# Performance work log

Hardware: AMD Instinct MI355X
Metric: run time of the kernel (lower is better)

The kernel has to match this reference:

```python
import jax, jax.numpy as jnp
import numpy as np

NUM_CLASS = 22  # restypes_with_x_and_gap: 20 AAs + 'X' + '-' (gap is last)


def layer_norm(x, g, b, eps=1e-5):
    mu = jnp.mean(x, axis=-1, keepdims=True)
    var = jnp.var(x, axis=-1, keepdims=True)
    return (x - mu) * jax.lax.rsqrt(var + eps) * g + b


def setup_inputs() -> dict:
    key = jax.random.key(0)
    ks = jax.random.split(key, 8)
    B, M, N, DS, DP = 1, 128, 256, 384, 128
    C = NUM_CLASS
    s = 0.02
    return dict(
        single=jax.random.normal(ks[0], (B, N, DS), dtype=jnp.float32),
        pair=jax.random.normal(ks[1], (B, N, N, DP), dtype=jnp.float32),
        msa=jax.random.randint(ks[2], (B, M, N), 0, C),
        w1=jax.random.normal(ks[3], (DS, DS), dtype=jnp.float32) * s,
        b1=jnp.zeros((DS,), jnp.float32),
        g1=jnp.ones((DS,), jnp.float32),
        be1=jnp.zeros((DS,), jnp.float32),
        w2=jax.random.normal(ks[4], (DS, C), dtype=jnp.float32) * s,
        b2=jnp.zeros((C,), jnp.float32),
        g2=jnp.ones((DP,), jnp.float32),
        be2=jnp.zeros((DP,), jnp.float32),
        w3=jax.random.normal(ks[5], (DP, C * C), dtype=jnp.float32) * s,
        b3=jnp.zeros((C * C,), jnp.float32),
    )


def reference(single, pair, msa, w1, b1, g1, be1, w2, b2, g2, be2, w3, b3):
    C = NUM_CLASS
    B, N = single.shape[0], single.shape[1]
    # make_mask(restypes_with_x_and_gap, '-'): 1 everywhere except the gap class (last index)
    label_mask = jnp.ones((C,), single.dtype).at[C - 1].set(0.0)

    # single branch: Linear -> GELU(exact) -> LayerNorm -> Linear
    h = jax.nn.gelu(single @ w1 + b1, approximate=False)
    ei = layer_norm(h, g1, be1) @ w2 + b2  # [B, N, C]

    # pairwise branch: symmetrize -> LayerNorm -> Linear -> ReLU, zero diagonal
    zsym = (pair + jnp.swapaxes(pair, 1, 2)) * 0.5
    eij = jax.nn.relu(layer_norm(zsym, g2, be2) @ w3 + b3)  # [B, N, N, C*C]
    eij = eij * (1.0 - jnp.eye(N, dtype=eij.dtype))[:, :, None]

    # coevolution logits: one-hot MSA (with gap class masked) contracted with pairwise couplings
    eijcd = eij.reshape(B, N, N, C, C)
    oh = jax.nn.one_hot(msa, C, dtype=eij.dtype) * label_mask  # [B, M, N, C] fold mask 'd' into one-hot
    hi = jnp.einsum('bmjd,bijcd->bmic', oh, eijcd)  # [B, M, N, C]
    logits = ei[:, None] + hi  # [B, M, N, C]
    return eij, ei, logits
```

## Files before the change

### kernel.cpp

```cpp
#include <hip/hip_runtime.h>
#include <hip/hip_bf16.h>

#define NN 256
#define MM 128
#define DS 384
#define DP 128
#define CC 22
#define C2 484

#define OUT_EI  (NN*NN*C2)
#define OUT_LOG (OUT_EI + NN*CC)

typedef __attribute__((ext_vector_type(8))) short short8;
typedef __attribute__((ext_vector_type(4))) float f32x4;

__device__ __forceinline__ unsigned f2bf(float x) {
  unsigned u = __float_as_uint(x);
  return (u + 0x7FFFu + ((u >> 16) & 1u)) >> 16;
}

__global__ void k_w3pack(const float* __restrict__ w3, int4* __restrict__ w3f) {
  int ct = blockIdx.x, kt = blockIdx.y, l = threadIdx.x;
  int c = ct * 16 + (l & 15);
  int kb = kt * 32 + (l >> 4) * 8;
  unsigned v[8];
#pragma unroll
  for (int e = 0; e < 8; ++e) {
    float x = (c < C2) ? w3[(kb + e) * C2 + c] : 0.f;
    v[e] = f2bf(x);
  }
  int4 pk;
  pk.x = (int)(v[0] | (v[1] << 16));
  pk.y = (int)(v[2] | (v[3] << 16));
  pk.z = (int)(v[4] | (v[5] << 16));
  pk.w = (int)(v[6] | (v[7] << 16));
  w3f[(kt * 31 + ct) * 64 + l] = pk;
}

__global__ void k_msat(const int* __restrict__ msa, unsigned char* __restrict__ mt) {
  int j = blockIdx.x, m = threadIdx.x;
  mt[j * MM + m] = (unsigned char)msa[m * NN + j];
}

__global__ __launch_bounds__(384) void k_single(
    const float* __restrict__ single, const float* __restrict__ w1,
    const float* __restrict__ b1, const float* __restrict__ g1,
    const float* __restrict__ be1, const float* __restrict__ w2,
    const float* __restrict__ b2, float* __restrict__ out_ei,
    float* __restrict__ out_log)
{
  __shared__ float srow[DS];
  __shared__ float hlx[DS];
  __shared__ float part[16 * CC];
  __shared__ float wred[8], wredq[8], mur[2];
  int n = blockIdx.x, t = threadIdx.x;
  srow[t] = single[n * DS + t];
  for (int idx = t; idx < MM * CC; idx += 384) {
    int m = idx / CC, c = idx - m * CC;
    out_log[(m * NN + n) * CC + c] = 0.f;
  }
  __syncthreads();
  float acc = b1[t];
#pragma unroll 8
  for (int d = 0; d < DS; ++d) acc = fmaf(srow[d], w1[d * DS + t], acc);
  float hv = 0.5f * acc * (1.0f + erff(acc * 0.70710678118654752f));
  float s = hv, q = hv * hv;
#pragma unroll
  for (int off = 32; off; off >>= 1) { s += __shfl_xor(s, off); q += __shfl_xor(q, off); }
  if ((t & 63) == 0) { wred[t >> 6] = s; wredq[t >> 6] = q; }
  __syncthreads();
  if (t == 0) {
    float S = 0.f, Q = 0.f;
    for (int w = 0; w < 6; ++w) { S += wred[w]; Q += wredq[w]; }
    float mu = S / (float)DS;
    mur[0] = mu; mur[1] = rsqrtf(Q / (float)DS - mu * mu + 1e-5f);
  }
  __syncthreads();
  hlx[t] = (hv - mur[0]) * mur[1] * g1[t] + be1[t];
  __syncthreads();
  if (t < 352) {
    int g = t / CC, c = t - g * CC;
    float p = 0.f;
#pragma unroll
    for (int k = g * 24; k < g * 24 + 24; ++k) p = fmaf(hlx[k], w2[k * CC + c], p);
    part[t] = p;
  }
  __syncthreads();
  if (t < CC) {
    float sm = b2[t];
#pragma unroll
    for (int g = 0; g < 16; ++g) sm += part[g * CC + t];
    out_ei[n * CC + t] = sm;
  }
}

__global__ __launch_bounds__(512, 4) void k_fused(
    const float* __restrict__ pair, const unsigned char* __restrict__ msa_tb,
    const float* __restrict__ g2, const float* __restrict__ be2,
    const float* __restrict__ b3, const int4* __restrict__ w3f,
    const float* __restrict__ ei,
    float* __restrict__ out_eij, float* __restrict__ out_log)
{
  __shared__ __align__(16) char smem[64512];
  unsigned char* msa_s = (unsigned char*)(smem + 52224);
  char* zln = smem + 56320;

  const int i = blockIdx.x, jh = blockIdx.y;
  const int t = threadIdx.x;
  const int w = t >> 6, l = t & 63;
  const int lr = l & 15, lg = l >> 4;

  for (int idx = t; idx < 52224 / 4; idx += 512) ((unsigned*)smem)[idx] = 0u;

  f32x4 acc[2];
  acc[0] = (f32x4){0.f, 0.f, 0.f, 0.f};
  acc[1] = (f32x4){0.f, 0.f, 0.f, 0.f};

  const float2 g2v = ((const float2*)g2)[l];
  const float2 bev = ((const float2*)be2)[l];
  const short8* w3fv = (const short8*)w3f;

  __syncthreads();

  for (int ch = 0; ch < 4; ++ch) {
    const int j0 = jh * 128 + ch * 32;

#pragma unroll
    for (int it = 0; it < 4; ++it) {
      int jl = w * 4 + it;
      int j = j0 + jl;
      float2 a = ((const float2*)(pair + (i * NN + j) * DP))[l];
      float2 b = ((const float2*)(pair + (j * NN + i) * DP))[l];
      float zx = 0.5f * (a.x + b.x), zy = 0.5f * (a.y + b.y);
      float s = zx + zy, q = zx * zx + zy * zy;
#pragma unroll
      for (int off = 32; off; off >>= 1) { s += __shfl_xor(s, off); q += __shfl_xor(q, off); }
      float mu = s * (1.f / 128.f);
      float rs = rsqrtf(q * (1.f / 128.f) - mu * mu + 1e-5f);
      float nx = (zx - mu) * rs * g2v.x + bev.x;
      float ny = (zy - mu) * rs * g2v.y + bev.y;
      unsigned pk = f2bf(nx) | (f2bf(ny) << 16);
      int blk = (l >> 2) ^ (jl & 15);
      *(unsigned*)(zln + jl * 256 + blk * 16 + (l & 3) * 4) = pk;
    }
    ((uint2*)msa_s)[t] = ((const uint2*)(msa_tb + j0 * MM))[t];
    __syncthreads();

    short8 a0[4], a1[4];
#pragma unroll
    for (int kt = 0; kt < 4; ++kt) {
      a0[kt] = *(const short8*)(zln + lr * 256 + (((kt * 4 + lg) ^ lr) * 16));
      a1[kt] = *(const short8*)(zln + (16 + lr) * 256 + (((kt * 4 + lg) ^ lr) * 16));
    }
    for (int ct = w; ct < 31; ct += 8) {
      f32x4 c0 = {0.f, 0.f, 0.f, 0.f}, c1 = {0.f, 0.f, 0.f, 0.f};
#pragma unroll
      for (int kt = 0; kt < 4; ++kt) {
        short8 bfr = w3fv[(kt * 31 + ct) * 64 + l];
        c0 = __builtin_amdgcn_mfma_f32_16x16x32_bf16(a0[kt], bfr, c0, 0, 0, 0);
        c1 = __builtin_amdgcn_mfma_f32_16x16x32_bf16(a1[kt], bfr, c1, 0, 0, 0);
      }
      int cflat = ct * 16 + lr;
      if (cflat < C2) {
        float bias = b3[cflat];
        int cdiv = cflat / CC;
        int dd = cflat - cdiv * CC;
#pragma unroll
        for (int r = 0; r < 4; ++r) {
          int jjl0 = lg * 4 + r;
          int j = j0 + jjl0;
          float v = fmaxf(c0[r] + bias, 0.f);
          if (j == i) v = 0.f;
          out_eij[(i * NN + j) * C2 + cflat] = v;
          *(unsigned short*)(smem + jjl0 * 1584 + cdiv * 72 + dd * 2) = (unsigned short)f2bf(v);

          int jjl1 = 16 + lg * 4 + r;
          j = j0 + jjl1;
          v = fmaxf(c1[r] + bias, 0.f);
          if (j == i) v = 0.f;
          out_eij[(i * NN + j) * C2 + cflat] = v;
          *(unsigned short*)(smem + jjl1 * 1584 + cdiv * 72 + dd * 2) = (unsigned short)f2bf(v);
        }
      }
    }
    __syncthreads();

    for (int jj = 0; jj < 32; ++jj) {
      int s = msa_s[jj * 128 + w * 16 + lr];
      int rel = s - lg * 8;
      unsigned hval = (s != 21 && ((unsigned)rel) < 8u) ? (0x3F80u << ((rel & 1) << 4)) : 0u;
      int word = rel >> 1;
      union { short8 s8; unsigned u[4]; } bu;
      bu.u[0] = (word == 0) ? hval : 0u;
      bu.u[1] = (word == 1) ? hval : 0u;
      bu.u[2] = (word == 2) ? hval : 0u;
      bu.u[3] = (word == 3) ? hval : 0u;
#pragma unroll
      for (int cp = 0; cp < 2; ++cp) {
        short8 af = *(const short8*)(smem + jj * 1584 + (cp * 16 + lr) * 72 + lg * 16);
        acc[cp] = __builtin_amdgcn_mfma_f32_16x16x32_bf16(af, bu.s8, acc[cp], 0, 0, 0);
      }
    }
    __syncthreads();
  }

  {
    int m = w * 16 + lr;
#pragma unroll
    for (int cp = 0; cp < 2; ++cp) {
#pragma unroll
      for (int r = 0; r < 4; ++r) {
        int c = cp * 16 + lg * 4 + r;
        if (c < CC) {
          float add = acc[cp][r] + (jh == 0 ? ei[i * CC + c] : 0.f);
          atomicAdd(&out_log[(m * NN + i) * CC + c], add);
        }
      }
    }
  }
}

extern "C" void kernel_launch(void* const* d_in, const int* in_sizes, int n_in,
                              void* d_out, int out_size, void* d_ws, size_t ws_size,
                              hipStream_t stream) {
  const float* single = (const float*)d_in[0];
  const float* pairp  = (const float*)d_in[1];
  const int*   msa    = (const int*)d_in[2];
  const float* w1  = (const float*)d_in[3];
  const float* b1  = (const float*)d_in[4];
  const float* g1  = (const float*)d_in[5];
  const float* be1 = (const float*)d_in[6];
  const float* w2  = (const float*)d_in[7];
  const float* b2  = (const float*)d_in[8];
  const float* g2  = (const float*)d_in[9];
  const float* be2 = (const float*)d_in[10];
  const float* w3  = (const float*)d_in[11];
  const float* b3  = (const float*)d_in[12];

  float* out = (float*)d_out;
  float* out_eij = out;
  float* out_ei  = out + OUT_EI;
  float* out_log = out + OUT_LOG;

  int4* w3f = (int4*)d_ws;
  unsigned char* msa_tb = (unsigned char*)d_ws + 131072;

  hipLaunchKernelGGL(k_w3pack, dim3(31, 4), dim3(64), 0, stream, w3, w3f);
  hipLaunchKernelGGL(k_msat, dim3(NN), dim3(MM), 0, stream, msa, msa_tb);
  hipLaunchKernelGGL(k_single, dim3(NN), dim3(384), 0, stream,
                     single, w1, b1, g1, be1, w2, b2, out_ei, out_log);
  hipLaunchKernelGGL(k_fused, dim3(256, 2), dim3(512), 0, stream,
                     pairp, msa_tb, g2, be2, b3, (const int4*)w3f,
                     out_ei, out_eij, out_log);
}
```

Measured before the change: 273.8 us.

## Split fused kernel into smaller 256-thread blocks over j quarters and merge prep kernels

The fused pairwise kernel now processes 32 j-columns per block in 16-row chunks with 4 waves, on a 256x8 grid instead of 256x2 with 512 threads. The eij staging buffer is compacted, and the einsum stage is reorganised so each wave covers two MSA row tiles. The w3 packing and MSA transpose kernels are merged into one launch. The aim is better occupancy, smaller LDS use and one fewer launch, at the cost of more atomic adds on the logits and fewer reuses of each w3 fragment per block.

```diff
diff --git a/kernel.cpp b/kernel.cpp
--- a/kernel.cpp
+++ b/kernel.cpp
@@ -11,6 +11,10 @@
 #define OUT_EI  (NN*NN*C2)
 #define OUT_LOG (OUT_EI + NN*CC)
 
+#define ZSTRJ 1056
+#define ZE_END (16*ZSTRJ + 512)
+#define LDS_TOTAL (ZE_END + 2048)
+
 typedef __attribute__((ext_vector_type(8))) short short8;
 typedef __attribute__((ext_vector_type(4))) float f32x4;
 
@@ -19,27 +23,27 @@
   return (u + 0x7FFFu + ((u >> 16) & 1u)) >> 16;
 }
 
-__global__ void k_w3pack(const float* __restrict__ w3, int4* __restrict__ w3f) {
-  int ct = blockIdx.x, kt = blockIdx.y, l = threadIdx.x;
-  int c = ct * 16 + (l & 15);
-  int kb = kt * 32 + (l >> 4) * 8;
-  unsigned v[8];
-#pragma unroll
-  for (int e = 0; e < 8; ++e) {
-    float x = (c < C2) ? w3[(kb + e) * C2 + c] : 0.f;
-    v[e] = f2bf(x);
-  }
-  int4 pk;
-  pk.x = (int)(v[0] | (v[1] << 16));
-  pk.y = (int)(v[2] | (v[3] << 16));
-  pk.z = (int)(v[4] | (v[5] << 16));
-  pk.w = (int)(v[6] | (v[7] << 16));
-  w3f[(kt * 31 + ct) * 64 + l] = pk;
-}
-
-__global__ void k_msat(const int* __restrict__ msa, unsigned char* __restrict__ mt) {
-  int j = blockIdx.x, m = threadIdx.x;
-  mt[j * MM + m] = (unsigned char)msa[m * NN + j];
+__global__ __launch_bounds__(128) void k_prep(
+    const float* __restrict__ w3, const int* __restrict__ msa,
+    int4* __restrict__ w3f, unsigned char* __restrict__ mt)
+{
+  int b = blockIdx.x, t = threadIdx.x;
+  mt[b * MM + t] = (unsigned char)msa[t * NN + b];
+  if (b < 124 && t < 64) {
+    int ct = b % 31, kt = b / 31, l = t;
+    int c = ct * 16 + (l & 15);
+    int kb = kt * 32 + (l >> 4) * 8;
+    unsigned v[8];
+#pragma unroll
+    for (int e = 0; e < 8; ++e)
+      v[e] = (c < C2) ? f2bf(w3[(kb + e) * C2 + c]) : 0u;
+    int4 pk;
+    pk.x = (int)(v[0] | (v[1] << 16));
+    pk.y = (int)(v[2] | (v[3] << 16));
+    pk.z = (int)(v[4] | (v[5] << 16));
+    pk.w = (int)(v[6] | (v[7] << 16));
+    w3f[(kt * 31 + ct) * 64 + l] = pk;
+  }
 }
 
 __global__ __launch_bounds__(384) void k_single(
@@ -94,36 +98,36 @@
   }
 }
 
-__global__ __launch_bounds__(512, 4) void k_fused(
+__global__ __launch_bounds__(256, 6) void k_fused(
     const float* __restrict__ pair, const unsigned char* __restrict__ msa_tb,
     const float* __restrict__ g2, const float* __restrict__ be2,
     const float* __restrict__ b3, const int4* __restrict__ w3f,
     const float* __restrict__ ei,
     float* __restrict__ out_eij, float* __restrict__ out_log)
 {
-  __shared__ __align__(16) char smem[64512];
-  unsigned char* msa_s = (unsigned char*)(smem + 52224);
-  char* zln = smem + 56320;
-
-  const int i = blockIdx.x, jh = blockIdx.y;
+  __shared__ __align__(16) char smem[LDS_TOTAL];
+  unsigned char* msa_s = (unsigned char*)(smem + ZE_END);
+
+  const int i = blockIdx.x, jq = blockIdx.y;
   const int t = threadIdx.x;
   const int w = t >> 6, l = t & 63;
   const int lr = l & 15, lg = l >> 4;
 
-  for (int idx = t; idx < 52224 / 4; idx += 512) ((unsigned*)smem)[idx] = 0u;
-
-  f32x4 acc[2];
-  acc[0] = (f32x4){0.f, 0.f, 0.f, 0.f};
-  acc[1] = (f32x4){0.f, 0.f, 0.f, 0.f};
+  for (int idx = t; idx < LDS_TOTAL / 4; idx += 256) ((unsigned*)smem)[idx] = 0u;
+
+  f32x4 acc[2][2];
+#pragma unroll
+  for (int a_ = 0; a_ < 2; ++a_)
+#pragma unroll
+    for (int b_ = 0; b_ < 2; ++b_) acc[a_][b_] = (f32x4){0.f, 0.f, 0.f, 0.f};
 
   const float2 g2v = ((const float2*)g2)[l];
   const float2 bev = ((const float2*)be2)[l];
   const short8* w3fv = (const short8*)w3f;
-
-  __syncthreads();
-
-  for (int ch = 0; ch < 4; ++ch) {
-    const int j0 = jh * 128 + ch * 32;
+  __syncthreads();
+
+  for (int ch = 0; ch < 2; ++ch) {
+    const int j0 = jq * 32 + ch * 16;
 
 #pragma unroll
     for (int it = 0; it < 4; ++it) {
@@ -140,26 +144,28 @@
       float nx = (zx - mu) * rs * g2v.x + bev.x;
       float ny = (zy - mu) * rs * g2v.y + bev.y;
       unsigned pk = f2bf(nx) | (f2bf(ny) << 16);
-      int blk = (l >> 2) ^ (jl & 15);
-      *(unsigned*)(zln + jl * 256 + blk * 16 + (l & 3) * 4) = pk;
+      int blk = (l >> 2) ^ jl;
+      *(unsigned*)(smem + jl * 256 + blk * 16 + (l & 3) * 4) = pk;
     }
     ((uint2*)msa_s)[t] = ((const uint2*)(msa_tb + j0 * MM))[t];
     __syncthreads();
 
-    short8 a0[4], a1[4];
-#pragma unroll
-    for (int kt = 0; kt < 4; ++kt) {
-      a0[kt] = *(const short8*)(zln + lr * 256 + (((kt * 4 + lg) ^ lr) * 16));
-      a1[kt] = *(const short8*)(zln + (16 + lr) * 256 + (((kt * 4 + lg) ^ lr) * 16));
-    }
-    for (int ct = w; ct < 31; ct += 8) {
-      f32x4 c0 = {0.f, 0.f, 0.f, 0.f}, c1 = {0.f, 0.f, 0.f, 0.f};
-#pragma unroll
-      for (int kt = 0; kt < 4; ++kt) {
-        short8 bfr = w3fv[(kt * 31 + ct) * 64 + l];
-        c0 = __builtin_amdgcn_mfma_f32_16x16x32_bf16(a0[kt], bfr, c0, 0, 0, 0);
-        c1 = __builtin_amdgcn_mfma_f32_16x16x32_bf16(a1[kt], bfr, c1, 0, 0, 0);
-      }
+    short8 afr[4];
+#pragma unroll
+    for (int kt = 0; kt < 4; ++kt)
+      afr[kt] = *(const short8*)(smem + lr * 256 + (((kt * 4 + lg) ^ lr) * 16));
+    __syncthreads();
+
+    for (int ct = w; ct < 31; ct += 4) {
+      short8 bf0 = w3fv[(0 * 31 + ct) * 64 + l];
+      short8 bf1 = w3fv[(1 * 31 + ct) * 64 + l];
+      short8 bf2 = w3fv[(2 * 31 + ct) * 64 + l];
+      short8 bf3 = w3fv[(3 * 31 + ct) * 64 + l];
+      f32x4 cc2 = {0.f, 0.f, 0.f, 0.f};
+      cc2 = __builtin_amdgcn_mfma_f32_16x16x32_bf16(afr[0], bf0, cc2, 0, 0, 0);
+      cc2 = __builtin_amdgcn_mfma_f32_16x16x32_bf16(afr[1], bf1, cc2, 0, 0, 0);
+      cc2 = __builtin_amdgcn_mfma_f32_16x16x32_bf16(afr[2], bf2, cc2, 0, 0, 0);
+      cc2 = __builtin_amdgcn_mfma_f32_16x16x32_bf16(afr[3], bf3, cc2, 0, 0, 0);
       int cflat = ct * 16 + lr;
       if (cflat < C2) {
         float bias = b3[cflat];
@@ -167,52 +173,59 @@
         int dd = cflat - cdiv * CC;
 #pragma unroll
         for (int r = 0; r < 4; ++r) {
-          int jjl0 = lg * 4 + r;
-          int j = j0 + jjl0;
-          float v = fmaxf(c0[r] + bias, 0.f);
+          int jl = lg * 4 + r, j = j0 + jl;
+          float v = fmaxf(cc2[r] + bias, 0.f);
           if (j == i) v = 0.f;
           out_eij[(i * NN + j) * C2 + cflat] = v;
-          *(unsigned short*)(smem + jjl0 * 1584 + cdiv * 72 + dd * 2) = (unsigned short)f2bf(v);
-
-          int jjl1 = 16 + lg * 4 + r;
-          j = j0 + jjl1;
-          v = fmaxf(c1[r] + bias, 0.f);
-          if (j == i) v = 0.f;
-          out_eij[(i * NN + j) * C2 + cflat] = v;
-          *(unsigned short*)(smem + jjl1 * 1584 + cdiv * 72 + dd * 2) = (unsigned short)f2bf(v);
+          *(unsigned short*)(smem + jl * ZSTRJ + cdiv * 48 + dd * 2) = (unsigned short)f2bf(v);
         }
       }
     }
     __syncthreads();
 
-    for (int jj = 0; jj < 32; ++jj) {
-      int s = msa_s[jj * 128 + w * 16 + lr];
-      int rel = s - lg * 8;
-      unsigned hval = (s != 21 && ((unsigned)rel) < 8u) ? (0x3F80u << ((rel & 1) << 4)) : 0u;
-      int word = rel >> 1;
-      union { short8 s8; unsigned u[4]; } bu;
-      bu.u[0] = (word == 0) ? hval : 0u;
-      bu.u[1] = (word == 1) ? hval : 0u;
-      bu.u[2] = (word == 2) ? hval : 0u;
-      bu.u[3] = (word == 3) ? hval : 0u;
+#pragma unroll 4
+    for (int jj = 0; jj < 16; ++jj) {
+      int s0 = msa_s[jj * 128 + w * 16 + lr];
+      int s1 = msa_s[jj * 128 + (w + 4) * 16 + lr];
+      union { short8 s8; unsigned u[4]; } b0, b1;
+      {
+        int rel = s0 - lg * 8;
+        unsigned hval = (s0 != 21 && ((unsigned)rel) < 8u) ? (0x3F80u << ((rel & 1) << 4)) : 0u;
+        int word = rel >> 1;
+        b0.u[0] = (word == 0) ? hval : 0u;
+        b0.u[1] = (word == 1) ? hval : 0u;
+        b0.u[2] = (word == 2) ? hval : 0u;
+        b0.u[3] = (word == 3) ? hval : 0u;
+      }
+      {
+        int rel = s1 - lg * 8;
+        unsigned hval = (s1 != 21 && ((unsigned)rel) < 8u) ? (0x3F80u << ((rel & 1) << 4)) : 0u;
+        int word = rel >> 1;
+        b1.u[0] = (word == 0) ? hval : 0u;
+        b1.u[1] = (word == 1) ? hval : 0u;
+        b1.u[2] = (word == 2) ? hval : 0u;
+        b1.u[3] = (word == 3) ? hval : 0u;
+      }
 #pragma unroll
       for (int cp = 0; cp < 2; ++cp) {
-        short8 af = *(const short8*)(smem + jj * 1584 + (cp * 16 + lr) * 72 + lg * 16);
-        acc[cp] = __builtin_amdgcn_mfma_f32_16x16x32_bf16(af, bu.s8, acc[cp], 0, 0, 0);
-      }
-    }
-    __syncthreads();
-  }
-
-  {
-    int m = w * 16 + lr;
+        short8 af = *(const short8*)(smem + jj * ZSTRJ + (cp * 16 + lr) * 48 + lg * 16);
+        acc[0][cp] = __builtin_amdgcn_mfma_f32_16x16x32_bf16(af, b0.s8, acc[0][cp], 0, 0, 0);
+        acc[1][cp] = __builtin_amdgcn_mfma_f32_16x16x32_bf16(af, b1.s8, acc[1][cp], 0, 0, 0);
+      }
+    }
+    __syncthreads();
+  }
+
+#pragma unroll
+  for (int mt = 0; mt < 2; ++mt) {
+    int m = (mt * 4 + w) * 16 + lr;
 #pragma unroll
     for (int cp = 0; cp < 2; ++cp) {
 #pragma unroll
       for (int r = 0; r < 4; ++r) {
         int c = cp * 16 + lg * 4 + r;
         if (c < CC) {
-          float add = acc[cp][r] + (jh == 0 ? ei[i * CC + c] : 0.f);
+          float add = acc[mt][cp][r] + (jq == 0 ? ei[i * CC + c] : 0.f);
           atomicAdd(&out_log[(m * NN + i) * CC + c], add);
         }
       }
@@ -245,11 +258,10 @@
   int4* w3f = (int4*)d_ws;
   unsigned char* msa_tb = (unsigned char*)d_ws + 131072;
 
-  hipLaunchKernelGGL(k_w3pack, dim3(31, 4), dim3(64), 0, stream, w3, w3f);
-  hipLaunchKernelGGL(k_msat, dim3(NN), dim3(MM), 0, stream, msa, msa_tb);
+  hipLaunchKernelGGL(k_prep, dim3(NN), dim3(128), 0, stream, w3, msa, w3f, msa_tb);
   hipLaunchKernelGGL(k_single, dim3(NN), dim3(384), 0, stream,
                      single, w1, b1, g1, be1, w2, b2, out_ei, out_log);
-  hipLaunchKernelGGL(k_fused, dim3(256, 2), dim3(512), 0, stream,
+  hipLaunchKernelGGL(k_fused, dim3(256, 8), dim3(256), 0, stream,
                      pairp, msa_tb, g2, be2, b3, (const int4*)w3f,
                      out_ei, out_eij, out_log);
 }
```

After: 396.4 us. 44.8% more time.

## Shrink fused-kernel LDS by aliasing staging buffers and merge prep kernels

Applied to the files above, without the earlier changes.

The fused kernel now reuses one LDS region for both the normalized pair tile and the bf16 coupling staging tile. A barrier after the A-fragment loads makes the reuse safe, and the coupling row stride drops from 72 to 48 bytes. Together these cut shared memory from about 64 KB to about 38 KB per block, so more blocks can fit on each CU. The two small prep kernels (w3 packing and MSA transpose) become one launch, the w3 fragment loads are hoisted ahead of the MFMAs, and the one-hot contraction loop is unrolled. The tighter stride means MFMA reads run past each valid row into neighbouring data. This relies on zero one-hot weights and discarded padding channels to stay correct.

```diff
diff --git a/kernel.cpp b/kernel.cpp
--- a/kernel.cpp
+++ b/kernel.cpp
@@ -11,6 +11,11 @@
 #define OUT_EI  (NN*NN*C2)
 #define OUT_LOG (OUT_EI + NN*CC)
 
+#define ZSTRJ 1056
+#define ZE_BYTES (32*ZSTRJ)
+#define ZE_END (ZE_BYTES + 512)
+#define LDS_TOTAL (ZE_END + 4096)
+
 typedef __attribute__((ext_vector_type(8))) short short8;
 typedef __attribute__((ext_vector_type(4))) float f32x4;
 
@@ -19,27 +24,27 @@
   return (u + 0x7FFFu + ((u >> 16) & 1u)) >> 16;
 }
 
-__global__ void k_w3pack(const float* __restrict__ w3, int4* __restrict__ w3f) {
-  int ct = blockIdx.x, kt = blockIdx.y, l = threadIdx.x;
-  int c = ct * 16 + (l & 15);
-  int kb = kt * 32 + (l >> 4) * 8;
-  unsigned v[8];
-#pragma unroll
-  for (int e = 0; e < 8; ++e) {
-    float x = (c < C2) ? w3[(kb + e) * C2 + c] : 0.f;
-    v[e] = f2bf(x);
-  }
-  int4 pk;
-  pk.x = (int)(v[0] | (v[1] << 16));
-  pk.y = (int)(v[2] | (v[3] << 16));
-  pk.z = (int)(v[4] | (v[5] << 16));
-  pk.w = (int)(v[6] | (v[7] << 16));
-  w3f[(kt * 31 + ct) * 64 + l] = pk;
-}
-
-__global__ void k_msat(const int* __restrict__ msa, unsigned char* __restrict__ mt) {
-  int j = blockIdx.x, m = threadIdx.x;
-  mt[j * MM + m] = (unsigned char)msa[m * NN + j];
+__global__ __launch_bounds__(128) void k_prep(
+    const float* __restrict__ w3, const int* __restrict__ msa,
+    int4* __restrict__ w3f, unsigned char* __restrict__ mt)
+{
+  int b = blockIdx.x, t = threadIdx.x;
+  mt[b * MM + t] = (unsigned char)msa[t * NN + b];
+  if (b < 124 && t < 64) {
+    int ct = b % 31, kt = b / 31, l = t;
+    int c = ct * 16 + (l & 15);
+    int kb = kt * 32 + (l >> 4) * 8;
+    unsigned v[8];
+#pragma unroll
+    for (int e = 0; e < 8; ++e)
+      v[e] = (c < C2) ? f2bf(w3[(kb + e) * C2 + c]) : 0u;
+    int4 pk;
+    pk.x = (int)(v[0] | (v[1] << 16));
+    pk.y = (int)(v[2] | (v[3] << 16));
+    pk.z = (int)(v[4] | (v[5] << 16));
+    pk.w = (int)(v[6] | (v[7] << 16));
+    w3f[(kt * 31 + ct) * 64 + l] = pk;
+  }
 }
 
 __global__ __launch_bounds__(384) void k_single(
@@ -101,16 +106,15 @@
     const float* __restrict__ ei,
     float* __restrict__ out_eij, float* __restrict__ out_log)
 {
-  __shared__ __align__(16) char smem[64512];
-  unsigned char* msa_s = (unsigned char*)(smem + 52224);
-  char* zln = smem + 56320;
+  __shared__ __align__(16) char smem[LDS_TOTAL];
+  unsigned char* msa_s = (unsigned char*)(smem + ZE_END);
 
   const int i = blockIdx.x, jh = blockIdx.y;
   const int t = threadIdx.x;
   const int w = t >> 6, l = t & 63;
   const int lr = l & 15, lg = l >> 4;
 
-  for (int idx = t; idx < 52224 / 4; idx += 512) ((unsigned*)smem)[idx] = 0u;
+  for (int idx = t; idx < LDS_TOTAL / 4; idx += 512) ((unsigned*)smem)[idx] = 0u;
 
   f32x4 acc[2];
   acc[0] = (f32x4){0.f, 0.f, 0.f, 0.f};
@@ -119,7 +123,6 @@
   const float2 g2v = ((const float2*)g2)[l];
   const float2 bev = ((const float2*)be2)[l];
   const short8* w3fv = (const short8*)w3f;
-
   __syncthreads();
 
   for (int ch = 0; ch < 4; ++ch) {
@@ -141,7 +144,7 @@
       float ny = (zy - mu) * rs * g2v.y + bev.y;
       unsigned pk = f2bf(nx) | (f2bf(ny) << 16);
       int blk = (l >> 2) ^ (jl & 15);
-      *(unsigned*)(zln + jl * 256 + blk * 16 + (l & 3) * 4) = pk;
+      *(unsigned*)(smem + jl * 256 + blk * 16 + (l & 3) * 4) = pk;
     }
     ((uint2*)msa_s)[t] = ((const uint2*)(msa_tb + j0 * MM))[t];
     __syncthreads();
@@ -149,17 +152,25 @@
     short8 a0[4], a1[4];
 #pragma unroll
     for (int kt = 0; kt < 4; ++kt) {
-      a0[kt] = *(const short8*)(zln + lr * 256 + (((kt * 4 + lg) ^ lr) * 16));
-      a1[kt] = *(const short8*)(zln + (16 + lr) * 256 + (((kt * 4 + lg) ^ lr) * 16));
-    }
+      a0[kt] = *(const short8*)(smem + lr * 256 + (((kt * 4 + lg) ^ lr) * 16));
+      a1[kt] = *(const short8*)(smem + (16 + lr) * 256 + (((kt * 4 + lg) ^ lr) * 16));
+    }
+    __syncthreads();
+
     for (int ct = w; ct < 31; ct += 8) {
+      short8 bf0 = w3fv[(0 * 31 + ct) * 64 + l];
+      short8 bf1 = w3fv[(1 * 31 + ct) * 64 + l];
+      short8 bf2 = w3fv[(2 * 31 + ct) * 64 + l];
+      short8 bf3 = w3fv[(3 * 31 + ct) * 64 + l];
       f32x4 c0 = {0.f, 0.f, 0.f, 0.f}, c1 = {0.f, 0.f, 0.f, 0.f};
-#pragma unroll
-      for (int kt = 0; kt < 4; ++kt) {
-        short8 bfr = w3fv[(kt * 31 + ct) * 64 + l];
-        c0 = __builtin_amdgcn_mfma_f32_16x16x32_bf16(a0[kt], bfr, c0, 0, 0, 0);
-        c1 = __builtin_amdgcn_mfma_f32_16x16x32_bf16(a1[kt], bfr, c1, 0, 0, 0);
-      }
+      c0 = __builtin_amdgcn_mfma_f32_16x16x32_bf16(a0[0], bf0, c0, 0, 0, 0);
+      c0 = __builtin_amdgcn_mfma_f32_16x16x32_bf16(a0[1], bf1, c0, 0, 0, 0);
+      c0 = __builtin_amdgcn_mfma_f32_16x16x32_bf16(a0[2], bf2, c0, 0, 0, 0);
+      c0 = __builtin_amdgcn_mfma_f32_16x16x32_bf16(a0[3], bf3, c0, 0, 0, 0);
+      c1 = __builtin_amdgcn_mfma_f32_16x16x32_bf16(a1[0], bf0, c1, 0, 0, 0);
+      c1 = __builtin_amdgcn_mfma_f32_16x16x32_bf16(a1[1], bf1, c1, 0, 0, 0);
+      c1 = __builtin_amdgcn_mfma_f32_16x16x32_bf16(a1[2], bf2, c1, 0, 0, 0);
+      c1 = __builtin_amdgcn_mfma_f32_16x16x32_bf16(a1[3], bf3, c1, 0, 0, 0);
       int cflat = ct * 16 + lr;
       if (cflat < C2) {
         float bias = b3[cflat];
@@ -167,24 +178,24 @@
         int dd = cflat - cdiv * CC;
 #pragma unroll
         for (int r = 0; r < 4; ++r) {
-          int jjl0 = lg * 4 + r;
-          int j = j0 + jjl0;
+          int jl0 = lg * 4 + r, j = j0 + jl0;
           float v = fmaxf(c0[r] + bias, 0.f);
           if (j == i) v = 0.f;
           out_eij[(i * NN + j) * C2 + cflat] = v;
-          *(unsigned short*)(smem + jjl0 * 1584 + cdiv * 72 + dd * 2) = (unsigned short)f2bf(v);
-
-          int jjl1 = 16 + lg * 4 + r;
-          j = j0 + jjl1;
+          *(unsigned short*)(smem + jl0 * ZSTRJ + cdiv * 48 + dd * 2) = (unsigned short)f2bf(v);
+
+          int jl1 = 16 + lg * 4 + r;
+          j = j0 + jl1;
           v = fmaxf(c1[r] + bias, 0.f);
           if (j == i) v = 0.f;
           out_eij[(i * NN + j) * C2 + cflat] = v;
-          *(unsigned short*)(smem + jjl1 * 1584 + cdiv * 72 + dd * 2) = (unsigned short)f2bf(v);
+          *(unsigned short*)(smem + jl1 * ZSTRJ + cdiv * 48 + dd * 2) = (unsigned short)f2bf(v);
         }
       }
     }
     __syncthreads();
 
+#pragma unroll 4
     for (int jj = 0; jj < 32; ++jj) {
       int s = msa_s[jj * 128 + w * 16 + lr];
       int rel = s - lg * 8;
@@ -197,7 +208,7 @@
       bu.u[3] = (word == 3) ? hval : 0u;
 #pragma unroll
       for (int cp = 0; cp < 2; ++cp) {
-        short8 af = *(const short8*)(smem + jj * 1584 + (cp * 16 + lr) * 72 + lg * 16);
+        short8 af = *(const short8*)(smem + jj * ZSTRJ + (cp * 16 + lr) * 48 + lg * 16);
         acc[cp] = __builtin_amdgcn_mfma_f32_16x16x32_bf16(af, bu.s8, acc[cp], 0, 0, 0);
       }
     }
@@ -245,8 +256,7 @@
   int4* w3f = (int4*)d_ws;
   unsigned char* msa_tb = (unsigned char*)d_ws + 131072;
 
-  hipLaunchKernelGGL(k_w3pack, dim3(31, 4), dim3(64), 0, stream, w3, w3f);
-  hipLaunchKernelGGL(k_msat, dim3(NN), dim3(MM), 0, stream, msa, msa_tb);
+  hipLaunchKernelGGL(k_prep, dim3(NN), dim3(128), 0, stream, w3, msa, w3f, msa_tb);
   hipLaunchKernelGGL(k_single, dim3(NN), dim3(384), 0, stream,
                      single, w1, b1, g1, be1, w2, b2, out_ei, out_log);
   hipLaunchKernelGGL(k_fused, dim3(256, 2), dim3(512), 0, stream,
```

Result: faster. 265.6 us (-3.0%).
